# Performance work log

Hardware: AMD Instinct MI355X
Metric: run time of the kernel (lower is better)

Reference implementation:

```python
import jax, jax.numpy as jnp
import numpy as np

L = 256  # hardcoded heatmap size in the original module
EPS = 1e-6
SIGMA = 1.0 / 3.0
BOX_T = 0.5
MASK_T = 0.1


def _gen_mask(Yp):
    """Faithful vectorized version of get_box_pos + make_heatmap for one [L,L] map."""
    M = jnp.where(Yp > BOX_T, Yp, 0.0)
    rows = jnp.sum(M, axis=1) > 0  # scan over rows (dim 0)
    cols = jnp.sum(M, axis=0) > 0  # scan over cols (dim 1)
    left = jnp.argmax(rows)                 # first nonzero row
    right = jnp.argmax(rows[::-1])          # offset of last nonzero row from the end
    up = jnp.argmax(cols)                   # first nonzero col
    down = jnp.argmax(cols[::-1])           # offset of last nonzero col from the end
    x_r = (right - left) // 2
    y_r = (down - up) // 2
    gt0 = (left + x_r).astype(jnp.float32)  # compared against coord0 = column index y
    gt1 = (up + y_r).astype(jnp.float32)    # compared against coord1 = row index x
    # make_heatmap: heatmap[x, y, :] = [y, x]
    ys = jnp.arange(L, dtype=jnp.float32)[None, :]  # coord0 over columns
    xs = jnp.arange(L, dtype=jnp.float32)[:, None]  # coord1 over rows
    d0 = (ys - gt0) / x_r.astype(jnp.float32)
    d1 = (xs - gt1) / y_r.astype(jnp.float32)
    h = d0 ** 4 + d1 ** 4                  # ((v^2)^2 summed over last dim)
    h = jnp.exp(-h / (2.0 * SIGMA) ** 2)
    return (h > MASK_T).astype(Yp.dtype)


def _per_sample(Yp, Yg):
    gen = _gen_mask(Yp)
    use_gt = jnp.max(Yg) > 0
    Yg_eff = jnp.where(use_gt, Yg, gen)
    positive = jnp.sum(Yg_eff * Yp)
    negative = jnp.sum((1.0 - Yg_eff) * Yp)
    return negative / (positive + EPS)


def setup_inputs() -> dict:
    key = jax.random.key(0)
    k1, k2, k3 = jax.random.split(key, 3)
    B = 512
    # predictions: background in [0, 0.4), a bright blob > 0.5 so box-finding works
    Y_pred = jax.random.uniform(k1, (B, L, L), dtype=jnp.float32) * 0.4
    blob = 0.6 + 0.4 * jax.random.uniform(k3, (B, 40, 80), dtype=jnp.float32)
    Y_pred = Y_pred.at[:, 100:140, 80:160].set(blob)
    # binary gt masks; zero out first half of batch to trigger the generated-mask branch
    Y_gt = (jax.random.uniform(k2, (B, L, L)) > 0.95).astype(jnp.float32)
    Y_gt = Y_gt.at[: B // 2].set(0.0)
    return {"Y_pred": Y_pred, "Y_gt": Y_gt}


def reference(Y_pred, Y_gt):
    ratios = jax.vmap(_per_sample)(Y_pred, Y_gt)  # [B]
    total = jnp.sum(ratios)
    N = Y_gt.shape[0]
    return jnp.where(total == 0, 0.0, jnp.log(total) / N)
```

## Files before the change

### kernel.cpp

```cpp
#include <hip/hip_runtime.h>
#include <math.h>

constexpr int L = 256;
constexpr float EPS = 1e-6f;
constexpr int REC_WORDS = 8;


typedef float f32x4 __attribute__((ext_vector_type(4)));

__device__ inline float wave_sum(float v) {
#pragma unroll
    for (int off = 32; off > 0; off >>= 1) v += __shfl_down(v, off, 64);
    return v;
}
__device__ inline int wave_min(int v) {
#pragma unroll
    for (int off = 32; off > 0; off >>= 1) v = min(v, __shfl_down(v, off, 64));
    return v;
}
__device__ inline int wave_max(int v) {
#pragma unroll
    for (int off = 32; off > 0; off >>= 1) v = max(v, __shfl_down(v, off, 64));
    return v;
}

__global__ __launch_bounds__(256) void pass1_kernel(
    const float* __restrict__ Yp, const float* __restrict__ Yg,
    unsigned* __restrict__ recs) {
    const int b = blockIdx.x >> 1;
    const int h = blockIdx.x & 1;
    const int t = threadIdx.x;
    const f32x4* yp4 = (const f32x4*)(Yp + (size_t)b * L * L) + h * 8192;
    const f32x4* yg4 = (const f32x4*)(Yg + (size_t)b * L * L) + h * 8192;
    unsigned* rec = recs + blockIdx.x * REC_WORDS;

    f32x4 Pc[4], Gc[4], Pn[4], Gn[4];
#pragma unroll
    for (int k = 0; k < 4; ++k) {
        Pc[k] = __builtin_nontemporal_load(yp4 + (k << 8) + t);
        Gc[k] = __builtin_nontemporal_load(yg4 + (k << 8) + t);
    }

    const int w = t >> 6;
    const int c0 = (t & 63) << 2;

    float sum_p = 0.f, sum_pg = 0.f;
    int anyg = 0;
    unsigned rowbits = 0u;
    unsigned cb0 = 0, cb1 = 0, cb2 = 0, cb3 = 0;
#pragma unroll
    for (int it = 0; it < 8; ++it) {
        if (it < 7) {
#pragma unroll
            for (int k = 0; k < 4; ++k) {
                const int off = ((it + 1) << 10) + (k << 8) + t;
                Pn[k] = __builtin_nontemporal_load(yp4 + off);
                Gn[k] = __builtin_nontemporal_load(yg4 + off);
            }
        }
#pragma unroll
        for (int k = 0; k < 4; ++k) {
            const f32x4 p = Pc[k], g = Gc[k];
            sum_p  += (p[0] + p[1]) + (p[2] + p[3]);
            sum_pg += p[0] * g[0] + p[1] * g[1] + p[2] * g[2] + p[3] * g[3];
            anyg |= (g[0] > 0.f) | (g[1] > 0.f) | (g[2] > 0.f) | (g[3] > 0.f);
            const unsigned bx = p[0] > 0.5f, by = p[1] > 0.5f,
                           bz = p[2] > 0.5f, bw = p[3] > 0.5f;
            rowbits |= (bx | by | bz | bw) << (it * 4 + k);
            cb0 |= bx; cb1 |= by; cb2 |= bz; cb3 |= bw;
        }
#pragma unroll
        for (int k = 0; k < 4; ++k) { Pc[k] = Pn[k]; Gc[k] = Gn[k]; }
    }

    int minr = 0x7FFFFFFF, maxr = -1, minc = 0x7FFFFFFF, maxc = -1;
    if (rowbits) {
        minr = h * 128 + w + 4 * __builtin_ctz(rowbits);
        maxr = h * 128 + w + 4 * (31 - __builtin_clz(rowbits));
        const unsigned colbits = cb0 | (cb1 << 1) | (cb2 << 2) | (cb3 << 3);
        minc = c0 + __builtin_ctz(colbits);
        maxc = c0 + (31 - __builtin_clz(colbits));
    }

    const int wave = t >> 6, lane = t & 63;
    const float wsp = wave_sum(sum_p);
    const float wspg = wave_sum(sum_pg);
    const int wanyg = __any(anyg);
    const int wminr = wave_min(minr), wmaxr = wave_max(maxr);
    const int wminc = wave_min(minc), wmaxc = wave_max(maxc);

    __shared__ float sh_p[4], sh_pg[4];
    __shared__ int sh_a[4], sh_minr[4], sh_maxr[4], sh_minc[4], sh_maxc[4];
    if (lane == 0) {
        sh_p[wave] = wsp; sh_pg[wave] = wspg; sh_a[wave] = wanyg;
        sh_minr[wave] = wminr; sh_maxr[wave] = wmaxr;
        sh_minc[wave] = wminc; sh_maxc[wave] = wmaxc;
    }
    __syncthreads();
    if (t == 0) {
        float sp = 0.f, spg = 0.f;
        int a = 0, mnr = 0x7FFFFFFF, mxr = -1, mnc = 0x7FFFFFFF, mxc = -1;
#pragma unroll
        for (int i = 0; i < 4; ++i) {
            sp += sh_p[i]; spg += sh_pg[i]; a |= sh_a[i];
            mnr = min(mnr, sh_minr[i]); mxr = max(mxr, sh_maxr[i]);
            mnc = min(mnc, sh_minc[i]); mxc = max(mxc, sh_maxc[i]);
        }
        ((float*)rec)[0] = sp;
        ((float*)rec)[1] = spg;
        rec[2] = (unsigned)a;
        ((int*)rec)[3] = mnr; ((int*)rec)[4] = mxr;
        ((int*)rec)[5] = mnc; ((int*)rec)[6] = mxc;
        rec[7] = 0u;
    }
}

__global__ __launch_bounds__(64) void pass2_kernel(
    const float* __restrict__ Yp, const unsigned* __restrict__ recs,
    float* __restrict__ ratios) {
    const int b = blockIdx.x;
    const int lane = threadIdx.x;
    const unsigned* r0 = recs + (2 * b + 0) * REC_WORDS;
    const unsigned* r1 = recs + (2 * b + 1) * REC_WORDS;
    const float* yp = Yp + (size_t)b * L * L;

    const float sum_p  = ((const float*)r0)[0] + ((const float*)r1)[0];
    const float sum_pg = ((const float*)r0)[1] + ((const float*)r1)[1];
    const unsigned anyg = r0[2] | r1[2];
    const int minr = min((int)r0[3], (int)r1[3]);
    const int maxr = max((int)r0[4], (int)r1[4]);
    const int minc = min((int)r0[5], (int)r1[5]);
    const int maxc = max((int)r0[6], (int)r1[6]);

    const bool any_r = maxr >= 0, any_c = maxc >= 0;
    const int left  = any_r ? minr : 0;
    const int right = any_r ? (L - 1 - maxr) : 0;
    const int up    = any_c ? minc : 0;
    const int down  = any_c ? (L - 1 - maxc) : 0;
    const int x_r = (right - left) >> 1;
    const int y_r = (down - up) >> 1;
    const float gt0 = (float)(left + x_r);
    const float gt1 = (float)(up + y_r);

    float positive;
    if (anyg) {
        positive = sum_pg;
    } else if (x_r == 0 || y_r == 0) {
        positive = 0.f;
    } else {
        const float inv_xr = 1.f / (float)x_r;
        const float inv_yr = 1.f / (float)y_r;
        const float mx = fabsf((float)x_r) * 1.02f + 1.f;
        const float my = fabsf((float)y_r) * 1.02f + 1.f;
        const int cl = max(0, (int)floorf(gt0 - mx));
        const int ch = min(L - 1, (int)ceilf(gt0 + mx));
        const int rl = max(0, (int)floorf(gt1 - my));
        const int rh = min(L - 1, (int)ceilf(gt1 + my));
        const int W = ch - cl + 1, H = rh - rl + 1;
        float pos = 0.f;
        for (int idx = lane; idx < W * H; idx += 64) {
            const int r = rl + idx / W;
            const int c = cl + idx % W;
            float d0 = ((float)c - gt0) * inv_xr;
            float d1 = ((float)r - gt1) * inv_yr;
            d0 *= d0; d0 *= d0;
            d1 *= d1; d1 *= d1;
            const float h = __expf(-2.25f * (d0 + d1));
            if (h > 0.1f) pos += yp[r * L + c];
        }
        positive = wave_sum(pos);
    }
    if (lane == 0) ratios[b] = (sum_p - positive) / (positive + EPS);
}

__global__ __launch_bounds__(256) void finalize_kernel(
    const float* __restrict__ ratios, float* __restrict__ out, int B) {
    float v = 0.f;
    for (int i = threadIdx.x; i < B; i += 256) v += ratios[i];
    v = wave_sum(v);
    __shared__ float part[4];
    const int wave = threadIdx.x >> 6, lane = threadIdx.x & 63;
    if (lane == 0) part[wave] = v;
    __syncthreads();
    if (threadIdx.x == 0) {
        const float total = part[0] + part[1] + part[2] + part[3];
        out[0] = (total == 0.f) ? 0.f : logf(total) / (float)B;
    }
}

extern "C" void kernel_launch(void* const* d_in, const int* in_sizes, int n_in,
                              void* d_out, int out_size, void* d_ws, size_t ws_size,
                              hipStream_t stream) {
    const float* Yp = (const float*)d_in[0];
    const float* Yg = (const float*)d_in[1];
    const int B = in_sizes[0] / (L * L);
    unsigned* recs = (unsigned*)d_ws;
    float* ratios = (float*)((char*)d_ws + (size_t)B * 2 * REC_WORDS * 4);
    pass1_kernel<<<B * 2, 256, 0, stream>>>(Yp, Yg, recs);
    pass2_kernel<<<B, 64, 0, stream>>>(Yp, recs, ratios);
    finalize_kernel<<<1, 256, 0, stream>>>(ratios, (float*)d_out, B);
}
```

Baseline: 261.4 us.

## Fuse box-finding and masked-sum passes into one per-sample kernel

Merges pass1 and pass2 into a single kernel with one 256-thread block per sample, so each block scans the whole map, builds the bounding box, then computes the generated-mask sum in place using all 256 threads. This drops a kernel launch and the intermediate record round-trip, and spreads the mask loop across four waves instead of one. In exchange the grid has half as many blocks (512) with longer per-block streaming, which may lower memory-level parallelism on a large GPU.

```diff
diff --git a/kernel.cpp b/kernel.cpp
--- a/kernel.cpp
+++ b/kernel.cpp
@@ -3,8 +3,6 @@
 
 constexpr int L = 256;
 constexpr float EPS = 1e-6f;
-constexpr int REC_WORDS = 8;
-
 
 typedef float f32x4 __attribute__((ext_vector_type(4)));
 
@@ -24,15 +22,14 @@
     return v;
 }
 
-__global__ __launch_bounds__(256) void pass1_kernel(
+__global__ __launch_bounds__(256) void sample_kernel(
     const float* __restrict__ Yp, const float* __restrict__ Yg,
-    unsigned* __restrict__ recs) {
-    const int b = blockIdx.x >> 1;
-    const int h = blockIdx.x & 1;
+    float* __restrict__ ratios) {
+    const int b = blockIdx.x;
     const int t = threadIdx.x;
-    const f32x4* yp4 = (const f32x4*)(Yp + (size_t)b * L * L) + h * 8192;
-    const f32x4* yg4 = (const f32x4*)(Yg + (size_t)b * L * L) + h * 8192;
-    unsigned* rec = recs + blockIdx.x * REC_WORDS;
+    const float* yp = Yp + (size_t)b * L * L;
+    const f32x4* yp4 = (const f32x4*)yp;
+    const f32x4* yg4 = (const f32x4*)(Yg + (size_t)b * L * L);
 
     f32x4 Pc[4], Gc[4], Pn[4], Gn[4];
 #pragma unroll
@@ -45,12 +42,12 @@
     const int c0 = (t & 63) << 2;
 
     float sum_p = 0.f, sum_pg = 0.f;
-    int anyg = 0;
-    unsigned rowbits = 0u;
+    int anyg_t = 0;
+    unsigned long long rowbits = 0ull;
     unsigned cb0 = 0, cb1 = 0, cb2 = 0, cb3 = 0;
 #pragma unroll
-    for (int it = 0; it < 8; ++it) {
-        if (it < 7) {
+    for (int it = 0; it < 16; ++it) {
+        if (it < 15) {
 #pragma unroll
             for (int k = 0; k < 4; ++k) {
                 const int off = ((it + 1) << 10) + (k << 8) + t;
@@ -63,10 +60,10 @@
             const f32x4 p = Pc[k], g = Gc[k];
             sum_p  += (p[0] + p[1]) + (p[2] + p[3]);
             sum_pg += p[0] * g[0] + p[1] * g[1] + p[2] * g[2] + p[3] * g[3];
-            anyg |= (g[0] > 0.f) | (g[1] > 0.f) | (g[2] > 0.f) | (g[3] > 0.f);
+            anyg_t |= (g[0] > 0.f) | (g[1] > 0.f) | (g[2] > 0.f) | (g[3] > 0.f);
             const unsigned bx = p[0] > 0.5f, by = p[1] > 0.5f,
                            bz = p[2] > 0.5f, bw = p[3] > 0.5f;
-            rowbits |= (bx | by | bz | bw) << (it * 4 + k);
+            rowbits |= (unsigned long long)(bx | by | bz | bw) << (it * 4 + k);
             cb0 |= bx; cb1 |= by; cb2 |= bz; cb3 |= bw;
         }
 #pragma unroll
@@ -75,8 +72,8 @@
 
     int minr = 0x7FFFFFFF, maxr = -1, minc = 0x7FFFFFFF, maxc = -1;
     if (rowbits) {
-        minr = h * 128 + w + 4 * __builtin_ctz(rowbits);
-        maxr = h * 128 + w + 4 * (31 - __builtin_clz(rowbits));
+        minr = w + 4 * __builtin_ctzll(rowbits);
+        maxr = w + 4 * (63 - __builtin_clzll(rowbits));
         const unsigned colbits = cb0 | (cb1 << 1) | (cb2 << 2) | (cb3 << 3);
         minc = c0 + __builtin_ctz(colbits);
         maxc = c0 + (31 - __builtin_clz(colbits));
@@ -85,7 +82,7 @@
     const int wave = t >> 6, lane = t & 63;
     const float wsp = wave_sum(sum_p);
     const float wspg = wave_sum(sum_pg);
-    const int wanyg = __any(anyg);
+    const int wanyg = __any(anyg_t);
     const int wminr = wave_min(minr), wmaxr = wave_max(maxr);
     const int wminc = wave_min(minc), wmaxc = wave_max(maxc);
 
@@ -97,57 +94,29 @@
         sh_minc[wave] = wminc; sh_maxc[wave] = wmaxc;
     }
     __syncthreads();
-    if (t == 0) {
-        float sp = 0.f, spg = 0.f;
-        int a = 0, mnr = 0x7FFFFFFF, mxr = -1, mnc = 0x7FFFFFFF, mxc = -1;
+
+    float sp = 0.f, spg = 0.f;
+    int anyg = 0, mnr = 0x7FFFFFFF, mxr = -1, mnc = 0x7FFFFFFF, mxc = -1;
 #pragma unroll
-        for (int i = 0; i < 4; ++i) {
-            sp += sh_p[i]; spg += sh_pg[i]; a |= sh_a[i];
-            mnr = min(mnr, sh_minr[i]); mxr = max(mxr, sh_maxr[i]);
-            mnc = min(mnc, sh_minc[i]); mxc = max(mxc, sh_maxc[i]);
-        }
-        ((float*)rec)[0] = sp;
-        ((float*)rec)[1] = spg;
-        rec[2] = (unsigned)a;
-        ((int*)rec)[3] = mnr; ((int*)rec)[4] = mxr;
-        ((int*)rec)[5] = mnc; ((int*)rec)[6] = mxc;
-        rec[7] = 0u;
+    for (int i = 0; i < 4; ++i) {
+        sp += sh_p[i]; spg += sh_pg[i]; anyg |= sh_a[i];
+        mnr = min(mnr, sh_minr[i]); mxr = max(mxr, sh_maxr[i]);
+        mnc = min(mnc, sh_minc[i]); mxc = max(mxc, sh_maxc[i]);
     }
-}
 
-__global__ __launch_bounds__(64) void pass2_kernel(
-    const float* __restrict__ Yp, const unsigned* __restrict__ recs,
-    float* __restrict__ ratios) {
-    const int b = blockIdx.x;
-    const int lane = threadIdx.x;
-    const unsigned* r0 = recs + (2 * b + 0) * REC_WORDS;
-    const unsigned* r1 = recs + (2 * b + 1) * REC_WORDS;
-    const float* yp = Yp + (size_t)b * L * L;
-
-    const float sum_p  = ((const float*)r0)[0] + ((const float*)r1)[0];
-    const float sum_pg = ((const float*)r0)[1] + ((const float*)r1)[1];
-    const unsigned anyg = r0[2] | r1[2];
-    const int minr = min((int)r0[3], (int)r1[3]);
-    const int maxr = max((int)r0[4], (int)r1[4]);
-    const int minc = min((int)r0[5], (int)r1[5]);
-    const int maxc = max((int)r0[6], (int)r1[6]);
-
-    const bool any_r = maxr >= 0, any_c = maxc >= 0;
-    const int left  = any_r ? minr : 0;
-    const int right = any_r ? (L - 1 - maxr) : 0;
-    const int up    = any_c ? minc : 0;
-    const int down  = any_c ? (L - 1 - maxc) : 0;
+    const bool any_r = mxr >= 0, any_c = mxc >= 0;
+    const int left  = any_r ? mnr : 0;
+    const int right = any_r ? (L - 1 - mxr) : 0;
+    const int up    = any_c ? mnc : 0;
+    const int down  = any_c ? (L - 1 - mxc) : 0;
     const int x_r = (right - left) >> 1;
     const int y_r = (down - up) >> 1;
     const float gt0 = (float)(left + x_r);
     const float gt1 = (float)(up + y_r);
 
-    float positive;
-    if (anyg) {
-        positive = sum_pg;
-    } else if (x_r == 0 || y_r == 0) {
-        positive = 0.f;
-    } else {
+    const bool gen = (!anyg) && (x_r != 0) && (y_r != 0);
+    float pos = 0.f;
+    if (gen) {
         const float inv_xr = 1.f / (float)x_r;
         const float inv_yr = 1.f / (float)y_r;
         const float mx = fabsf((float)x_r) * 1.02f + 1.f;
@@ -157,8 +126,7 @@
         const int rl = max(0, (int)floorf(gt1 - my));
         const int rh = min(L - 1, (int)ceilf(gt1 + my));
         const int W = ch - cl + 1, H = rh - rl + 1;
-        float pos = 0.f;
-        for (int idx = lane; idx < W * H; idx += 64) {
+        for (int idx = t; idx < W * H; idx += 256) {
             const int r = rl + idx / W;
             const int c = cl + idx % W;
             float d0 = ((float)c - gt0) * inv_xr;
@@ -168,9 +136,16 @@
             const float h = __expf(-2.25f * (d0 + d1));
             if (h > 0.1f) pos += yp[r * L + c];
         }
-        positive = wave_sum(pos);
     }
-    if (lane == 0) ratios[b] = (sum_p - positive) / (positive + EPS);
+    __syncthreads();
+    const float wpos = wave_sum(pos);
+    if (lane == 0) sh_p[wave] = wpos;
+    __syncthreads();
+    if (t == 0) {
+        const float posg = sh_p[0] + sh_p[1] + sh_p[2] + sh_p[3];
+        const float positive = anyg ? spg : (gen ? posg : 0.f);
+        ratios[b] = (sp - positive) / (positive + EPS);
+    }
 }
 
 __global__ __launch_bounds__(256) void finalize_kernel(
@@ -194,9 +169,7 @@
     const float* Yp = (const float*)d_in[0];
     const float* Yg = (const float*)d_in[1];
     const int B = in_sizes[0] / (L * L);
-    unsigned* recs = (unsigned*)d_ws;
-    float* ratios = (float*)((char*)d_ws + (size_t)B * 2 * REC_WORDS * 4);
-    pass1_kernel<<<B * 2, 256, 0, stream>>>(Yp, Yg, recs);
-    pass2_kernel<<<B, 64, 0, stream>>>(Yp, recs, ratios);
+    float* ratios = (float*)d_ws;
+    sample_kernel<<<B, 256, 0, stream>>>(Yp, Yg, ratios);
     finalize_kernel<<<1, 256, 0, stream>>>(ratios, (float*)d_out, B);
 }
```

Result: slower. 336.9 us (+28.9%).
